# Optimization experiments

Measured on AMD Instinct MI355X. Metric: run time of the kernel, lower is better.

Reference implementation:

```python
import jax, jax.numpy as jnp
import numpy as np

ALPHA = 0.2  # LeakyReLU negative slope
NEG_INF = -9e15  # matches torch's -9e15 mask value


def gat_head(h, mask, W, a):
    # h: [N, Fin], W: [Fin, Fout], a: [2*Fout]
    # Faithful to torch GraphAttentionLayer but WITHOUT materializing the
    # N x N x 2F pairwise concat: a^T [Wh_i ; Wh_j] = (Wh_i . a1) + (Wh_j . a2).
    Wh = h @ W                                  # [N, F]
    F = W.shape[1]
    f = Wh @ a[:F]                              # [N] source term
    g = Wh @ a[F:]                              # [N] target term
    e = jax.nn.leaky_relu(f[:, None] + g[None, :], ALPHA)  # [N, N]
    e = jnp.where(mask, e, NEG_INF)
    attn = jax.nn.softmax(e, axis=1)            # row-wise softmax over neighbors
    return jax.nn.elu(attn @ Wh)                # [N, F]


def multi_head_gat(x, mask, W_heads, a_heads, W_out, a_out):
    # W_heads: [H, Fin, F], a_heads: [H, 2F]; concat heads then out-attention.
    heads = jax.vmap(gat_head, in_axes=(None, None, 0, 0))(x, mask, W_heads, a_heads)  # [H, N, F]
    N = x.shape[0]
    x = jnp.transpose(heads, (1, 0, 2)).reshape(N, -1)  # [N, H*F]
    # dropout(p=0.1) is identity in eval mode; elu applied twice as in torch code
    return jax.nn.elu(gat_head(x, mask, W_out, a_out))


def setup_inputs() -> dict:
    key = jax.random.key(0)
    ks = jax.random.split(key, 10)
    T, N, Din, H, Fh, L = 32, 512, 3, 8, 256, 3
    pose = jax.random.normal(ks[0], (T, N, Din), dtype=jnp.float32)
    adj = (jax.random.uniform(ks[1], (N, N)) < 0.06).astype(jnp.int32)
    adj = jnp.maximum(adj, jnp.eye(N, dtype=jnp.int32))
    s = 0.05  # xavier-ish scale, keeps logits stable
    return {
        "pose_sequence": pose,
        "adjacency_matrix": adj,
        "Wp": jax.random.normal(ks[2], (Din, Fh), jnp.float32) * s,
        "bp": jnp.zeros((Fh,), jnp.float32),
        "W_heads": jax.random.normal(ks[3], (L, H, Fh, Fh), jnp.float32) * s,
        "a_heads": jax.random.normal(ks[4], (L, H, 2 * Fh), jnp.float32) * s,
        "W_out": jax.random.normal(ks[5], (L, H * Fh, Fh), jnp.float32) * s,
        "a_out": jax.random.normal(ks[6], (L, 2 * Fh), jnp.float32) * s,
        "Wo": jax.random.normal(ks[7], (Fh, Fh), jnp.float32) * s,
        "bo": jnp.zeros((Fh,), jnp.float32),
    }


def reference(pose_sequence, adjacency_matrix, Wp, bp, W_heads, a_heads, W_out, a_out, Wo, bo):
    mask = adjacency_matrix > 0  # [N, N] bool
    n_layers = W_heads.shape[0]

    def frame(p):  # p: [N, Din]
        x = p @ Wp + bp  # input projection -> [N, Fh]
        for l in range(n_layers):
            x = multi_head_gat(x, mask, W_heads[l], a_heads[l], W_out[l], a_out[l])
        return x.mean(0) @ Wo + bo  # per-frame pooled output [Fh]

    return jax.vmap(frame)(pose_sequence)  # [T, Fh]
```

## Files before the change

### kernel.cpp

```cpp
#include <hip/hip_runtime.h>
#include <hip/hip_fp16.h>
#include <cstdint>
#include <cstddef>


typedef _Float16 f16x2 __attribute__((ext_vector_type(2)));
typedef _Float16 f16x8 __attribute__((ext_vector_type(8)));
typedef float f32x4 __attribute__((ext_vector_type(4)));
typedef unsigned int uint32;

__device__ __forceinline__ void async_copy16(const void* g, void* l) {
    __builtin_amdgcn_global_load_lds(
        (const __attribute__((address_space(1))) void*)g,
        (__attribute__((address_space(3))) void*)l, 16, 0, 0);
}
__device__ __forceinline__ float fast_elu(float v) {
    return v > 0.f ? v : (__expf(v) - 1.f);
}
__device__ __forceinline__ unsigned short f2h(float f) {
    return __builtin_bit_cast(unsigned short, (_Float16)f);
}
__device__ __forceinline__ float h2f(unsigned short u) {
    return (float)__builtin_bit_cast(_Float16, u);
}

__global__ __launch_bounds__(256)
void build_csr_kernel(const int* __restrict__ adj, int* __restrict__ cnt,
                      int* __restrict__ idxout)
{
    int row  = blockIdx.x * 4 + (threadIdx.x >> 6);
    int lane = threadIdx.x & 63;
    if (row >= 512) return;
    int base = 0;
    for (int j0 = 0; j0 < 512; j0 += 64) {
        int j = j0 + lane;
        bool pred = adj[row * 512 + j] > 0;
        unsigned long long m = __ballot(pred);
        if (pred) {
            int pos = __popcll(m & ((1ull << lane) - 1ull));
            idxout[row * 512 + base + pos] = j;
        }
        base += __popcll(m);
    }
    int s = base + lane;
    if (s < 64) idxout[row * 512 + s] = 0;
    if (lane == 0) cnt[row] = base;
}

__global__ __launch_bounds__(256)
void transpose_f16_kernel(const float* __restrict__ in,
                          unsigned short* __restrict__ ob, int K, int N)
{
    int b = blockIdx.z;
    int k0 = blockIdx.y * 32, n0 = blockIdx.x * 32;
    __shared__ float tile[32][33];
    int tx = threadIdx.x & 31, ty = threadIdx.x >> 5;
    const float* inb = in + (size_t)b * K * N;
    #pragma unroll
    for (int r = 0; r < 32; r += 8)
        tile[ty + r][tx] = inb[(size_t)(k0 + ty + r) * N + n0 + tx];
    __syncthreads();
    unsigned short* obb = ob + (size_t)b * K * N;
    #pragma unroll
    for (int r = 0; r < 32; r += 8)
        obb[(size_t)(n0 + ty + r) * K + k0 + tx] = f2h(tile[tx][ty + r]);
}

__global__ __launch_bounds__(256)
void w12_kernel(const float* __restrict__ W, const float* __restrict__ a,
                float* __restrict__ w1, float* __restrict__ w2)
{
    int b = blockIdx.x, k = threadIdx.x;
    const float* Wb = W + (size_t)b * 256 * 256 + (size_t)k * 256;
    const float* ab = a + (size_t)b * 512;
    float s1 = 0.f, s2 = 0.f;
    for (int n = 0; n < 256; ++n) {
        float w = Wb[n];
        s1 = fmaf(w, ab[n], s1);
        s2 = fmaf(w, ab[256 + n], s2);
    }
    w1[b * 256 + k] = s1;
    w2[b * 256 + k] = s2;
}

__global__ __launch_bounds__(256)
void proj_fg_kernel(const float* __restrict__ pose, const float* __restrict__ Wp,
                    const float* __restrict__ bp,
                    const float* __restrict__ w1, const float* __restrict__ w2,
                    unsigned short* __restrict__ xH,
                    float* __restrict__ fbuf, float* __restrict__ gbuf)
{
    int w = threadIdx.x >> 6, lane = threadIdx.x & 63;
    int row = blockIdx.x * 4 + w;
    float p0 = pose[row * 3 + 0], p1 = pose[row * 3 + 1], p2 = pose[row * 3 + 2];
    int c4 = lane * 4;
    float4 w0v = *(const float4*)&Wp[0 * 256 + c4];
    float4 w1v_ = *(const float4*)&Wp[1 * 256 + c4];
    float4 w2v_ = *(const float4*)&Wp[2 * 256 + c4];
    float4 bv = *(const float4*)&bp[c4];
    float4 xv;
    xv.x = fmaf(p0, w0v.x, fmaf(p1, w1v_.x, fmaf(p2, w2v_.x, bv.x)));
    xv.y = fmaf(p0, w0v.y, fmaf(p1, w1v_.y, fmaf(p2, w2v_.y, bv.y)));
    xv.z = fmaf(p0, w0v.z, fmaf(p1, w1v_.z, fmaf(p2, w2v_.z, bv.z)));
    xv.w = fmaf(p0, w0v.w, fmaf(p1, w1v_.w, fmaf(p2, w2v_.w, bv.w)));
    ushort4 b4 = {f2h(xv.x), f2h(xv.y), f2h(xv.z), f2h(xv.w)};
    *(ushort4*)&xH[(size_t)row * 256 + c4] = b4;

    float sf[8], sg[8];
    #pragma unroll
    for (int h = 0; h < 8; ++h) {
        float4 a1 = *(const float4*)&w1[h * 256 + c4];
        float4 a2 = *(const float4*)&w2[h * 256 + c4];
        sf[h] = xv.x * a1.x + xv.y * a1.y + xv.z * a1.z + xv.w * a1.w;
        sg[h] = xv.x * a2.x + xv.y * a2.y + xv.z * a2.z + xv.w * a2.w;
    }
    #pragma unroll
    for (int off = 32; off > 0; off >>= 1)
        #pragma unroll
        for (int h = 0; h < 8; ++h) {
            sf[h] += __shfl_xor(sf[h], off);
            sg[h] += __shfl_xor(sg[h], off);
        }
    if (lane == 0) {
        float4 a = {sf[0], sf[1], sf[2], sf[3]}, b = {sf[4], sf[5], sf[6], sf[7]};
        float4 c = {sg[0], sg[1], sg[2], sg[3]}, d = {sg[4], sg[5], sg[6], sg[7]};
        *(float4*)&fbuf[(size_t)row * 8]     = a;
        *(float4*)&fbuf[(size_t)row * 8 + 4] = b;
        *(float4*)&gbuf[(size_t)row * 8]     = c;
        *(float4*)&gbuf[(size_t)row * 8 + 4] = d;
    }
}

__global__ __launch_bounds__(256)
void gemm_mfma_kernel(const unsigned short* __restrict__ A,
                      const unsigned short* __restrict__ B,
                      unsigned short* __restrict__ partB,
                      unsigned short* __restrict__ outB,
                      int M, int N, int Kld, int Klen,
                      long strideAz, long strideBz, long strideCz,
                      int outStride, int colOffZ)
{
    int z = blockIdx.z;
    const unsigned short* az = A + (size_t)z * strideAz;
    const unsigned short* bz = B + (size_t)z * strideBz;
    int m0 = blockIdx.y * 64, n0 = blockIdx.x * 128;

    __shared__ __align__(16) unsigned short lsA[2 * 64 * 32];
    __shared__ __align__(16) unsigned short lsB[2 * 128 * 32];

    int tid = threadIdx.x, w = tid >> 6, lane = tid & 63;
    int qr = w >> 1, qc = w & 1;
    int l15 = lane & 15, kgp = lane >> 4;

    f32x4 acc[2][4];
    #pragma unroll
    for (int i = 0; i < 2; i++)
        #pragma unroll
        for (int j = 0; j < 4; j++)
            acc[i][j] = (f32x4){0.f, 0.f, 0.f, 0.f};

    for (int k0 = 0; k0 < Klen; k0 += 64) {
        __syncthreads();
        #pragma unroll
        for (int cc = 0; cc < 6; ++cc) {
            int chunk = w * 6 + cc;
            if (chunk < 8) {
                int pp = chunk >> 2, lc = chunk & 3;
                int g = lc * 64 + lane;
                int row = g >> 2;
                int kg = (g & 3) ^ ((row + (row >> 2)) & 3);
                async_copy16(az + (size_t)(m0 + row) * Kld + k0 + pp * 32 + kg * 8,
                             &lsA[pp * 2048 + (size_t)g * 8]);
            } else {
                int bc = chunk - 8;
                int pp = bc >> 3, lc = bc & 7;
                int g = lc * 64 + lane;
                int row = g >> 2;
                int kg = (g & 3) ^ ((row + (row >> 2)) & 3);
                async_copy16(bz + (size_t)(n0 + row) * Kld + k0 + pp * 32 + kg * 8,
                             &lsB[pp * 4096 + (size_t)g * 8]);
            }
        }
        __syncthreads();

        #pragma unroll
        for (int pp = 0; pp < 2; ++pp) {
            f16x8 fa[2], fb[4];
            #pragma unroll
            for (int tr = 0; tr < 2; ++tr) {
                int row = qr * 32 + tr * 16 + l15;
                int cell = row * 4 + (kgp ^ ((row + (row >> 2)) & 3));
                fa[tr] = *(const f16x8*)&lsA[pp * 2048 + cell * 8];
            }
            #pragma unroll
            for (int tc = 0; tc < 4; ++tc) {
                int nn = qc * 64 + tc * 16 + l15;
                int cell = nn * 4 + (kgp ^ ((nn + (nn >> 2)) & 3));
                fb[tc] = *(const f16x8*)&lsB[pp * 4096 + cell * 8];
            }
            #pragma unroll
            for (int tr = 0; tr < 2; ++tr)
                #pragma unroll
                for (int tc = 0; tc < 4; ++tc)
                    acc[tr][tc] = __builtin_amdgcn_mfma_f32_16x16x32_f16(
                        fa[tr], fb[tc], acc[tr][tc], 0, 0, 0);
        }
    }
    if (outB) {
        #pragma unroll
        for (int tr = 0; tr < 2; ++tr) {
            int rbase = m0 + qr * 32 + tr * 16 + (lane >> 4) * 4;
            #pragma unroll
            for (int tc = 0; tc < 4; ++tc) {
                int col = z * colOffZ + n0 + qc * 64 + tc * 16 + l15;
                #pragma unroll
                for (int r = 0; r < 4; ++r) {
                    float o = fast_elu(acc[tr][tc][r]);
                    outB[(size_t)(rbase + r) * outStride + col] = f2h(o);
                }
            }
        }
    } else {
        unsigned short* Cz = partB + (size_t)z * strideCz;
        #pragma unroll
        for (int tr = 0; tr < 2; ++tr) {
            int rbase = m0 + qr * 32 + tr * 16 + (lane >> 4) * 4;
            #pragma unroll
            for (int tc = 0; tc < 4; ++tc) {
                int col = n0 + qc * 64 + tc * 16 + l15;
                #pragma unroll
                for (int r = 0; r < 4; ++r)
                    Cz[(size_t)(rbase + r) * N + col] = f2h(acc[tr][tc][r]);
            }
        }
    }
}

__global__ __launch_bounds__(256)
void reduce_fg_kernel(const unsigned short* __restrict__ part, long partStride,
                      const float* __restrict__ a,
                      unsigned short* __restrict__ whoH,
                      float* __restrict__ fAll, float* __restrict__ gAll, int R)
{
    int row = blockIdx.x * 4 + (threadIdx.x >> 6);
    int lane = threadIdx.x & 63;
    const unsigned short* p0 = part + (size_t)row * 256 + lane * 4;
    ushort4 u0 = *(const ushort4*)p0;
    ushort4 u1 = *(const ushort4*)(p0 + partStride);
    float4 v = {h2f(u0.x) + h2f(u1.x), h2f(u0.y) + h2f(u1.y),
                h2f(u0.z) + h2f(u1.z), h2f(u0.w) + h2f(u1.w)};
    ushort4 b4 = {f2h(v.x), f2h(v.y), f2h(v.z), f2h(v.w)};
    *(ushort4*)&whoH[(size_t)row * 256 + lane * 4] = b4;
    float4 a1 = *(const float4*)&a[lane * 4];
    float4 a2 = *(const float4*)&a[256 + lane * 4];
    float sf = v.x * a1.x + v.y * a1.y + v.z * a1.z + v.w * a1.w;
    float sg = v.x * a2.x + v.y * a2.y + v.z * a2.z + v.w * a2.w;
    #pragma unroll
    for (int off = 32; off > 0; off >>= 1) {
        sf += __shfl_down(sf, off);
        sg += __shfl_down(sg, off);
    }
    if (lane == 0) { fAll[row] = sf; gAll[row] = sg; }
}

__global__ __launch_bounds__(256)
void attn_heads_kernel(const unsigned short* __restrict__ xH,
                       const float* __restrict__ fbuf, const float* __restrict__ gbuf,
                       const int* __restrict__ nbr_cnt, const int* __restrict__ nbr_idx,
                       unsigned short* __restrict__ yH, int R)
{
    __shared__ uint32 ppk[4][32][8];
    int t = blockIdx.y;
    int w = threadIdx.x >> 6;
    int i = blockIdx.x * 4 + w;
    int lane = threadIdx.x & 63;
    int jc = nbr_cnt[i];
    jc = jc < 64 ? jc : 64;
    int row = t * 512 + i;
    const unsigned short* xt = xH + (size_t)t * 512 * 256;

    float4 fA = *(const float4*)&fbuf[(size_t)row * 8];
    float4 fB = *(const float4*)&fbuf[(size_t)row * 8 + 4];

    bool ok = lane < jc;
    float4 gA = {0.f, 0.f, 0.f, 0.f}, gB = {0.f, 0.f, 0.f, 0.f};
    if (ok) {
        int id = nbr_idx[i * 512 + lane];
        const float* gp = &gbuf[(size_t)(t * 512 + id) * 8];
        gA = *(const float4*)gp;
        gB = *(const float4*)(gp + 4);
    }
    float e[8] = {fA.x + gA.x, fA.y + gA.y, fA.z + gA.z, fA.w + gA.w,
                  fB.x + gB.x, fB.y + gB.y, fB.z + gB.z, fB.w + gB.w};
    float p[8];
    #pragma unroll
    for (int h = 0; h < 8; ++h) {
        float eh = e[h] >= 0.f ? e[h] : 0.2f * e[h];
        float pe = ok ? __expf(eh) : 0.f;
        float s = pe;
        #pragma unroll
        for (int off = 32; off > 0; off >>= 1) s += __shfl_xor(s, off);
        p[h] = pe * (1.f / s);
    }
    uint32 u[8];
    #pragma unroll
    for (int h = 0; h < 8; ++h) {
        float pn = __shfl_xor(p[h], 1);
        u[h] = (uint32)f2h(p[h]) | ((uint32)f2h(pn) << 16);
    }
    if (!(lane & 1)) {
        int q = lane >> 1;
        uint4 lo = {u[0], u[1], u[2], u[3]}, hi = {u[4], u[5], u[6], u[7]};
        *(uint4*)&ppk[w][q][0] = lo;
        *(uint4*)&ppk[w][q][4] = hi;
    }

    const int* nl = nbr_idx + (size_t)__builtin_amdgcn_readfirstlane(i) * 512;
    int np = (jc + 1) >> 1;
    float4 acc[8];
    #pragma unroll
    for (int h = 0; h < 8; ++h) acc[h] = (float4){0.f, 0.f, 0.f, 0.f};
    int f4 = lane * 4;
    #pragma unroll 4
    for (int q = 0; q < np; ++q) {
        int ia = nl[2 * q], ib = nl[2 * q + 1];
        uint4 plo = *(const uint4*)&ppk[w][q][0];
        uint4 phi = *(const uint4*)&ppk[w][q][4];
        uint2 xa = *(const uint2*)&xt[(size_t)ia * 256 + f4];
        uint2 xb = *(const uint2*)&xt[(size_t)ib * 256 + f4];
        uint32 pr0 = __builtin_amdgcn_perm(xb.x, xa.x, 0x05040100u);
        uint32 pr1 = __builtin_amdgcn_perm(xb.x, xa.x, 0x07060302u);
        uint32 pr2 = __builtin_amdgcn_perm(xb.y, xa.y, 0x05040100u);
        uint32 pr3 = __builtin_amdgcn_perm(xb.y, xa.y, 0x07060302u);
        f16x2 c0 = __builtin_bit_cast(f16x2, pr0);
        f16x2 c1 = __builtin_bit_cast(f16x2, pr1);
        f16x2 c2 = __builtin_bit_cast(f16x2, pr2);
        f16x2 c3 = __builtin_bit_cast(f16x2, pr3);
        uint32 pw[8] = {plo.x, plo.y, plo.z, plo.w, phi.x, phi.y, phi.z, phi.w};
        #pragma unroll
        for (int h = 0; h < 8; ++h) {
            f16x2 ph = __builtin_bit_cast(f16x2, pw[h]);
            acc[h].x = __builtin_amdgcn_fdot2(c0, ph, acc[h].x, false);
            acc[h].y = __builtin_amdgcn_fdot2(c1, ph, acc[h].y, false);
            acc[h].z = __builtin_amdgcn_fdot2(c2, ph, acc[h].z, false);
            acc[h].w = __builtin_amdgcn_fdot2(c3, ph, acc[h].w, false);
        }
    }

    #pragma unroll
    for (int h = 0; h < 8; ++h) {
        ushort4 b4 = {f2h(acc[h].x), f2h(acc[h].y), f2h(acc[h].z), f2h(acc[h].w)};
        size_t ob = (size_t)h * R * 256 + (size_t)row * 256 + f4;
        *(ushort4*)&yH[ob] = b4;
    }
}

__global__ __launch_bounds__(256)
void attn_out_kernel(const unsigned short* __restrict__ whoH,
                     const float* __restrict__ fAll, const float* __restrict__ gAll,
                     const int* __restrict__ nbr_cnt, const int* __restrict__ nbr_idx,
                     unsigned short* __restrict__ xH,
                     const float* __restrict__ w1n, const float* __restrict__ w2n,
                     float* __restrict__ fbuf, float* __restrict__ gbuf)
{
    __shared__ uint32 pp2[4][32];
    int t = blockIdx.y;
    int w = threadIdx.x >> 6;
    int i = blockIdx.x * 4 + w;
    int lane = threadIdx.x & 63;
    const unsigned short* whF = whoH + (size_t)t * 512 * 256;
    int jc = nbr_cnt[i];
    jc = jc < 64 ? jc : 64;

    float fi = fAll[t * 512 + i];
    const float* g = gAll + t * 512;
    bool ok = lane < jc;
    float p = 0.f;
    if (ok) {
        int id = nbr_idx[i * 512 + lane];
        float ee = fi + g[id];
        float e2 = ee >= 0.f ? ee : 0.2f * ee;
        p = __expf(e2);
    }
    float s = p;
    #pragma unroll
    for (int off = 32; off > 0; off >>= 1) s += __shfl_xor(s, off);
    p *= (1.f / s);
    float pn = __shfl_xor(p, 1);
    if (!(lane & 1))
        pp2[w][lane >> 1] = (uint32)f2h(p) | ((uint32)f2h(pn) << 16);

    const int* nl = nbr_idx + (size_t)__builtin_amdgcn_readfirstlane(i) * 512;
    int np = (jc + 1) >> 1;
    float4 acc = {0.f, 0.f, 0.f, 0.f};
    int f4 = lane * 4;
    #pragma unroll 4
    for (int q = 0; q < np; ++q) {
        int ia = nl[2 * q], ib = nl[2 * q + 1];
        f16x2 ph = __builtin_bit_cast(f16x2, pp2[w][q]);
        uint2 xa = *(const uint2*)&whF[(size_t)ia * 256 + f4];
        uint2 xb = *(const uint2*)&whF[(size_t)ib * 256 + f4];
        uint32 pr0 = __builtin_amdgcn_perm(xb.x, xa.x, 0x05040100u);
        uint32 pr1 = __builtin_amdgcn_perm(xb.x, xa.x, 0x07060302u);
        uint32 pr2 = __builtin_amdgcn_perm(xb.y, xa.y, 0x05040100u);
        uint32 pr3 = __builtin_amdgcn_perm(xb.y, xa.y, 0x07060302u);
        acc.x = __builtin_amdgcn_fdot2(__builtin_bit_cast(f16x2, pr0), ph, acc.x, false);
        acc.y = __builtin_amdgcn_fdot2(__builtin_bit_cast(f16x2, pr1), ph, acc.y, false);
        acc.z = __builtin_amdgcn_fdot2(__builtin_bit_cast(f16x2, pr2), ph, acc.z, false);
        acc.w = __builtin_amdgcn_fdot2(__builtin_bit_cast(f16x2, pr3), ph, acc.w, false);
    }
    float o[4] = {acc.x, acc.y, acc.z, acc.w};
    #pragma unroll
    for (int k = 0; k < 4; ++k)
        o[k] = fast_elu(fast_elu(o[k]));
    float4 ov = {o[0], o[1], o[2], o[3]};
    int row = t * 512 + i;
    ushort4 b4 = {f2h(ov.x), f2h(ov.y), f2h(ov.z), f2h(ov.w)};
    *(ushort4*)&xH[(size_t)row * 256 + f4] = b4;

    if (w1n) {
        float sf[8], sg[8];
        #pragma unroll
        for (int h = 0; h < 8; ++h) {
            float4 w1v = *(const float4*)&w1n[h * 256 + f4];
            float4 w2v = *(const float4*)&w2n[h * 256 + f4];
            sf[h] = ov.x * w1v.x + ov.y * w1v.y + ov.z * w1v.z + ov.w * w1v.w;
            sg[h] = ov.x * w2v.x + ov.y * w2v.y + ov.z * w2v.z + ov.w * w2v.w;
        }
        #pragma unroll
        for (int off = 32; off > 0; off >>= 1)
            #pragma unroll
            for (int h = 0; h < 8; ++h) {
                sf[h] += __shfl_xor(sf[h], off);
                sg[h] += __shfl_xor(sg[h], off);
            }
        if (lane == 0) {
            float4 a = {sf[0], sf[1], sf[2], sf[3]}, b = {sf[4], sf[5], sf[6], sf[7]};
            float4 cc = {sg[0], sg[1], sg[2], sg[3]}, d = {sg[4], sg[5], sg[6], sg[7]};
            *(float4*)&fbuf[(size_t)row * 8]     = a;
            *(float4*)&fbuf[(size_t)row * 8 + 4] = b;
            *(float4*)&gbuf[(size_t)row * 8]     = cc;
            *(float4*)&gbuf[(size_t)row * 8 + 4] = d;
        }
    }
}

__global__ __launch_bounds__(256)
void final_kernel(const unsigned short* __restrict__ xH, const float* __restrict__ Wo,
                  const float* __restrict__ bo, float* __restrict__ out)
{
    int t = blockIdx.x, c = threadIdx.x;
    __shared__ float pooled[256];
    float s = 0.f;
    const unsigned short* xt = xH + (size_t)t * 512 * 256;
    for (int n = 0; n < 512; ++n) s += h2f(xt[(size_t)n * 256 + c]);
    pooled[c] = s * (1.f / 512.f);
    __syncthreads();
    float o = bo[c];
    for (int k = 0; k < 256; k++) o = fmaf(pooled[k], Wo[k * 256 + c], o);
    out[t * 256 + c] = o;
}

extern "C" void kernel_launch(void* const* d_in, const int* in_sizes, int n_in,
                              void* d_out, int out_size, void* d_ws, size_t ws_size,
                              hipStream_t stream)
{
    const float* pose   = (const float*)d_in[0];
    const int*   adj    = (const int*)  d_in[1];
    const float* Wp     = (const float*)d_in[2];
    const float* bp     = (const float*)d_in[3];
    const float* Wh_w   = (const float*)d_in[4];
    const float* a_h    = (const float*)d_in[5];
    const float* W_outw = (const float*)d_in[6];
    const float* a_o    = (const float*)d_in[7];
    const float* Wo     = (const float*)d_in[8];
    const float* bo     = (const float*)d_in[9];
    float* out = (float*)d_out;

    const int T = 32, N = 512, F = 256, H = 8, L = 3, Din = 3;

    auto align256 = [](size_t b) { return (b + 255) & ~(size_t)255; };
    auto need = [&](int TC) -> size_t {
        size_t R = (size_t)TC * N;
        size_t b = 0;
        b += align256(R * F * 2);
        b += align256((size_t)H * R * F * 2);
        b += align256(R * (size_t)H * F * 2);
        b += align256(2 * R * F * 2);
        b += align256(R * F * 2);
        b += 2 * align256(R * 8 * 4);
        b += 2 * align256(R * 4);
        b += 2 * align256((size_t)L * H * F * F * 2);
        b += 2 * align256((size_t)L * H * F * 4);
        b += align256(512 * 4) + align256(512 * 512 * 4);
        return b + 4096;
    };
    int TC = 32;
    while (TC > 1 && need(TC) > ws_size) TC >>= 1;
    size_t R = (size_t)TC * N;

    char* wp = (char*)d_ws;
    auto alloc = [&](size_t bytes) -> char* {
        char* r = wp; wp += (bytes + 255) & ~(size_t)255; return r;
    };
    unsigned short* xB     = (unsigned short*)alloc(R * F * 2);
    unsigned short* yB     = (unsigned short*)alloc((size_t)H * R * F * 2);
    unsigned short* xcatB  = (unsigned short*)alloc(R * (size_t)H * F * 2);
    unsigned short* partBf = (unsigned short*)alloc(2 * R * F * 2);
    unsigned short* whoB   = (unsigned short*)alloc(R * F * 2);
    float*          fbuf   = (float*)alloc(R * 8 * 4);
    float*          gbuf   = (float*)alloc(R * 8 * 4);
    float*          fAll   = (float*)alloc(R * 4);
    float*          gAll   = (float*)alloc(R * 4);
    unsigned short* wtb    = (unsigned short*)alloc((size_t)L * H * F * F * 2);
    unsigned short* wotb   = (unsigned short*)alloc((size_t)L * H * F * F * 2);
    float*          w1     = (float*)alloc((size_t)L * H * F * 4);
    float*          w2     = (float*)alloc((size_t)L * H * F * 4);
    int*            ncnt   = (int*)alloc(512 * 4);
    int*            nidx   = (int*)alloc(512 * 512 * 4);

    build_csr_kernel<<<128, 256, 0, stream>>>(adj, ncnt, nidx);
    transpose_f16_kernel<<<dim3(F / 32, F / 32, L * H), 256, 0, stream>>>(
        Wh_w, wtb, F, F);
    transpose_f16_kernel<<<dim3(F / 32, (H * F) / 32, L), 256, 0, stream>>>(
        W_outw, wotb, H * F, F);
    w12_kernel<<<L * H, 256, 0, stream>>>(Wh_w, a_h, w1, w2);

    for (int t0 = 0; t0 < T; t0 += TC) {
        proj_fg_kernel<<<(unsigned)(R / 4), 256, 0, stream>>>(
            pose + (size_t)t0 * N * Din, Wp, bp, w1, w2, xB, fbuf, gbuf);

        for (int l = 0; l < L; l++) {
            attn_heads_kernel<<<dim3(128, TC), 256, 0, stream>>>(
                xB, fbuf, gbuf, ncnt, nidx, yB, (int)R);
            gemm_mfma_kernel<<<dim3(F / 128, (unsigned)(R / 64), H), 256, 0, stream>>>(
                yB, wtb + (size_t)l * H * F * F,
                nullptr, xcatB,
                (int)R, F, F, F,
                (long)R * F, (long)F * F, 0, H * F, F);
            gemm_mfma_kernel<<<dim3(F / 128, (unsigned)(R / 64), 2), 256, 0, stream>>>(
                xcatB, wotb + (size_t)l * H * F * F,
                partBf, nullptr,
                (int)R, F, H * F, H * F / 2,
                (long)(H * F / 2), (long)(H * F / 2), (long)R * F, 0, 0);
            reduce_fg_kernel<<<(unsigned)(R / 4), 256, 0, stream>>>(
                partBf, (long)R * F, a_o + (size_t)l * 2 * F, whoB, fAll, gAll, (int)R);
            const float* w1n = (l + 1 < L) ? w1 + (size_t)(l + 1) * H * F : nullptr;
            const float* w2n = (l + 1 < L) ? w2 + (size_t)(l + 1) * H * F : nullptr;
            attn_out_kernel<<<dim3(128, TC), 256, 0, stream>>>(
                whoB, fAll, gAll, ncnt, nidx, xB, w1n, w2n, fbuf, gbuf);
        }
        final_kernel<<<TC, 256, 0, stream>>>(xB, Wo, bo, out + (size_t)t0 * F);
    }
}
```

Before: 574.8 us.

## Rewrite per-head attention aggregation as one-row-per-block MFMA with LDS-staged neighbors

After: 660.9 us. +15.0%, slower.

```diff
diff --git a/kernel.cpp b/kernel.cpp
--- a/kernel.cpp
+++ b/kernel.cpp
@@ -269,90 +269,85 @@
                        const int* __restrict__ nbr_cnt, const int* __restrict__ nbr_idx,
                        unsigned short* __restrict__ yH, int R)
 {
-    __shared__ uint32 ppk[4][32][8];
-    int t = blockIdx.y;
-    int w = threadIdx.x >> 6;
-    int i = blockIdx.x * 4 + w;
-    int lane = threadIdx.x & 63;
+    __shared__ __align__(16) unsigned short Xg[64][256];
+    __shared__ __align__(16) unsigned short pl[64][16];
+    __shared__ __align__(16) unsigned short yT[8][256];
+
+    int t = blockIdx.y, i = blockIdx.x;
+    int tid = threadIdx.x, w = tid >> 6, L = tid & 63;
     int jc = nbr_cnt[i];
     jc = jc < 64 ? jc : 64;
-    int row = t * 512 + i;
     const unsigned short* xt = xH + (size_t)t * 512 * 256;
-
-    float4 fA = *(const float4*)&fbuf[(size_t)row * 8];
-    float4 fB = *(const float4*)&fbuf[(size_t)row * 8 + 4];
-
-    bool ok = lane < jc;
-    float4 gA = {0.f, 0.f, 0.f, 0.f}, gB = {0.f, 0.f, 0.f, 0.f};
-    if (ok) {
-        int id = nbr_idx[i * 512 + lane];
-        const float* gp = &gbuf[(size_t)(t * 512 + id) * 8];
-        gA = *(const float4*)gp;
-        gB = *(const float4*)(gp + 4);
-    }
-    float e[8] = {fA.x + gA.x, fA.y + gA.y, fA.z + gA.z, fA.w + gA.w,
-                  fB.x + gB.x, fB.y + gB.y, fB.z + gB.z, fB.w + gB.w};
-    float p[8];
-    #pragma unroll
-    for (int h = 0; h < 8; ++h) {
-        float eh = e[h] >= 0.f ? e[h] : 0.2f * e[h];
-        float pe = ok ? __expf(eh) : 0.f;
-        float s = pe;
-        #pragma unroll
-        for (int off = 32; off > 0; off >>= 1) s += __shfl_xor(s, off);
-        p[h] = pe * (1.f / s);
-    }
-    uint32 u[8];
-    #pragma unroll
-    for (int h = 0; h < 8; ++h) {
-        float pn = __shfl_xor(p[h], 1);
-        u[h] = (uint32)f2h(p[h]) | ((uint32)f2h(pn) << 16);
-    }
-    if (!(lane & 1)) {
-        int q = lane >> 1;
-        uint4 lo = {u[0], u[1], u[2], u[3]}, hi = {u[4], u[5], u[6], u[7]};
-        *(uint4*)&ppk[w][q][0] = lo;
-        *(uint4*)&ppk[w][q][4] = hi;
-    }
-
-    const int* nl = nbr_idx + (size_t)__builtin_amdgcn_readfirstlane(i) * 512;
-    int np = (jc + 1) >> 1;
-    float4 acc[8];
-    #pragma unroll
-    for (int h = 0; h < 8; ++h) acc[h] = (float4){0.f, 0.f, 0.f, 0.f};
-    int f4 = lane * 4;
-    #pragma unroll 4
-    for (int q = 0; q < np; ++q) {
-        int ia = nl[2 * q], ib = nl[2 * q + 1];
-        uint4 plo = *(const uint4*)&ppk[w][q][0];
-        uint4 phi = *(const uint4*)&ppk[w][q][4];
-        uint2 xa = *(const uint2*)&xt[(size_t)ia * 256 + f4];
-        uint2 xb = *(const uint2*)&xt[(size_t)ib * 256 + f4];
-        uint32 pr0 = __builtin_amdgcn_perm(xb.x, xa.x, 0x05040100u);
-        uint32 pr1 = __builtin_amdgcn_perm(xb.x, xa.x, 0x07060302u);
-        uint32 pr2 = __builtin_amdgcn_perm(xb.y, xa.y, 0x05040100u);
-        uint32 pr3 = __builtin_amdgcn_perm(xb.y, xa.y, 0x07060302u);
-        f16x2 c0 = __builtin_bit_cast(f16x2, pr0);
-        f16x2 c1 = __builtin_bit_cast(f16x2, pr1);
-        f16x2 c2 = __builtin_bit_cast(f16x2, pr2);
-        f16x2 c3 = __builtin_bit_cast(f16x2, pr3);
-        uint32 pw[8] = {plo.x, plo.y, plo.z, plo.w, phi.x, phi.y, phi.z, phi.w};
-        #pragma unroll
-        for (int h = 0; h < 8; ++h) {
-            f16x2 ph = __builtin_bit_cast(f16x2, pw[h]);
-            acc[h].x = __builtin_amdgcn_fdot2(c0, ph, acc[h].x, false);
-            acc[h].y = __builtin_amdgcn_fdot2(c1, ph, acc[h].y, false);
-            acc[h].z = __builtin_amdgcn_fdot2(c2, ph, acc[h].z, false);
-            acc[h].w = __builtin_amdgcn_fdot2(c3, ph, acc[h].w, false);
-        }
-    }
-
-    #pragma unroll
-    for (int h = 0; h < 8; ++h) {
-        ushort4 b4 = {f2h(acc[h].x), f2h(acc[h].y), f2h(acc[h].z), f2h(acc[h].w)};
-        size_t ob = (size_t)h * R * 256 + (size_t)row * 256 + f4;
-        *(ushort4*)&yH[ob] = b4;
-    }
+    const int* nrow = nbr_idx + i * 512;
+
+    int id0 = nrow[L];
+    #pragma unroll
+    for (int m = 0; m < 8; ++m) {
+        int rw = 16 * w + 2 * m + (L >> 5);
+        int idg = __shfl(id0, rw);
+        async_copy16(xt + (size_t)idg * 256 + (L & 31) * 8,
+                     &Xg[0][0] + (size_t)(16 * w + 2 * m) * 256 + (size_t)L * 8);
+    }
+
+    bool ok = L < jc;
+    float2 fv = *(const float2*)&fbuf[(size_t)(t * 512 + i) * 8 + 2 * w];
+    float2 gv = *(const float2*)&gbuf[(size_t)(t * 512 + id0) * 8 + 2 * w];
+    float e0 = fv.x + gv.x, e1 = fv.y + gv.y;
+    e0 = e0 >= 0.f ? e0 : 0.2f * e0;
+    e1 = e1 >= 0.f ? e1 : 0.2f * e1;
+    float p0 = ok ? __expf(e0) : 0.f;
+    float p1 = ok ? __expf(e1) : 0.f;
+    float s0 = p0, s1 = p1;
+    #pragma unroll
+    for (int off = 32; off > 0; off >>= 1) {
+        s0 += __shfl_xor(s0, off);
+        s1 += __shfl_xor(s1, off);
+    }
+    p0 *= (1.f / s0);
+    p1 *= (1.f / s1);
+    uint32 pk = (uint32)f2h(p0) | ((uint32)f2h(p1) << 16);
+    *(uint32*)&pl[L][2 * w] = pk;
+    if (w == 0) { uint4 z4 = {0, 0, 0, 0}; *(uint4*)&pl[L][8] = z4; }
+
+    __syncthreads();
+
+    int l15 = L & 15, g4 = L >> 4;
+    f16x8 af[2];
+    #pragma unroll
+    for (int kt = 0; kt < 2; ++kt)
+        #pragma unroll
+        for (int jj = 0; jj < 8; ++jj)
+            af[kt][jj] = __builtin_bit_cast(_Float16, pl[kt * 32 + g4 * 8 + jj][l15]);
+
+    f32x4 acc[4];
+    #pragma unroll
+    for (int nt = 0; nt < 4; ++nt) acc[nt] = (f32x4){0.f, 0.f, 0.f, 0.f};
+    #pragma unroll
+    for (int nt = 0; nt < 4; ++nt) {
+        int n0 = w * 64 + nt * 16;
+        #pragma unroll
+        for (int kt = 0; kt < 2; ++kt) {
+            f16x8 bf;
+            #pragma unroll
+            for (int jj = 0; jj < 8; ++jj)
+                bf[jj] = __builtin_bit_cast(_Float16, Xg[kt * 32 + g4 * 8 + jj][n0 + l15]);
+            acc[nt] = __builtin_amdgcn_mfma_f32_16x16x32_f16(af[kt], bf, acc[nt], 0, 0, 0);
+        }
+    }
+    if (g4 < 2) {
+        #pragma unroll
+        for (int nt = 0; nt < 4; ++nt) {
+            int col = w * 64 + nt * 16 + l15;
+            #pragma unroll
+            for (int r = 0; r < 4; ++r)
+                yT[g4 * 4 + r][col] = f2h(acc[nt][r]);
+        }
+    }
+    __syncthreads();
+
+    int h = tid >> 5, c8 = (tid & 31) * 8;
+    size_t ob = (size_t)h * R * 256 + (size_t)(t * 512 + i) * 256 + c8;
+    *(uint4*)&yH[ob] = *(const uint4*)&yT[h][c8];
 }
 
 __global__ __launch_bounds__(256)
@@ -375,12 +370,13 @@
     float fi = fAll[t * 512 + i];
     const float* g = gAll + t * 512;
     bool ok = lane < jc;
+    int id = 0;
     float p = 0.f;
     if (ok) {
-        int id = nbr_idx[i * 512 + lane];
+        id = nbr_idx[i * 512 + lane];
         float ee = fi + g[id];
-        float e2 = ee >= 0.f ? ee : 0.2f * ee;
-        p = __expf(e2);
+        float e = ee >= 0.f ? ee : 0.2f * ee;
+        p = __expf(e);
     }
     float s = p;
     #pragma unroll
@@ -531,7 +527,7 @@
             pose + (size_t)t0 * N * Din, Wp, bp, w1, w2, xB, fbuf, gbuf);
 
         for (int l = 0; l < L; l++) {
-            attn_heads_kernel<<<dim3(128, TC), 256, 0, stream>>>(
+            attn_heads_kernel<<<dim3(512, TC), 256, 0, stream>>>(
                 xB, fbuf, gbuf, ncnt, nidx, yB, (int)R);
             gemm_mfma_kernel<<<dim3(F / 128, (unsigned)(R / 64), H), 256, 0, stream>>>(
                 yB, wtb + (size_t)l * H * F * F,
```
